# Performance work log

Measured on AMD Instinct MI355X. Metric: run time of the kernel, lower is better.

## Reference

```python
import jax, jax.numpy as jnp
import numpy as np

HEADS = 8
DK = 64            # key_size == size_per_head
NEIGHBORS = 3
KSIZE = 1 + 2 * NEIGHBORS  # 7 (rate=1)


def setup_inputs() -> dict:
    key = jax.random.key(0)
    k1, k2, k3, k4 = jax.random.split(key, 4)
    B, HW, S, D = 2, 64, 256, 512
    inputs = jax.random.normal(k1, (B, HW, S, D), dtype=jnp.float32)
    pos_bias = jax.random.normal(k2, (HEADS, S, KSIZE), dtype=jnp.float32)
    W_qkv = jax.random.normal(k3, (D, 3 * HEADS * DK), dtype=jnp.float32) * 0.02
    W_out = jax.random.normal(k4, (HEADS * DK, D), dtype=jnp.float32) * 0.02
    return {"inputs": inputs, "pos_bias": pos_bias, "W_qkv": W_qkv, "W_out": W_out}


def reference(inputs, pos_bias, W_qkv, W_out):
    B, HW, S, D = inputs.shape
    # qkv projection (no bias), split into q, k, v
    qkv = inputs @ W_qkv                                   # [B,HW,S,3*H*DK]
    q, k, v = jnp.split(qkv, 3, axis=-1)
    q = (q / jnp.sqrt(jnp.float32(DK))).reshape(B, HW, S, HEADS, DK)
    k = k.reshape(B, HW, S, HEADS, DK)
    v = v.reshape(B, HW, S, HEADS, DK)

    # zero-pad keys/values along seq (faithful to F.pad with value=0)
    pad = NEIGHBORS
    kp = jnp.pad(k, ((0, 0), (0, 0), (pad, pad), (0, 0), (0, 0)))
    vp = jnp.pad(v, ((0, 0), (0, 0), (pad, pad), (0, 0), (0, 0)))

    # sliding-window gather: window w for query i covers padded positions i..i+KSIZE-1
    idx = jnp.arange(S)[:, None] + jnp.arange(KSIZE)[None, :]  # [S,KSIZE]
    kw = kp[:, :, idx]                                         # [B,HW,S,KSIZE,H,DK]
    vw = vp[:, :, idx]                                         # [B,HW,S,KSIZE,H,DK]

    # scores over the window
    attn = jnp.einsum('bnshd,bnswhd->bnswh', q, kw)            # [B,HW,S,KSIZE,H]
    # additive positional bias: [H,S,KSIZE] -> [S,KSIZE,H] broadcast
    attn = attn + jnp.transpose(pos_bias, (1, 2, 0))[None, None]
    attn = jax.nn.softmax(attn, axis=-2)                       # softmax over window dim

    out = jnp.einsum('bnswh,bnswhd->bnshd', attn, vw)          # [B,HW,S,H,DK]
    out = out.reshape(B, HW, S, HEADS * DK)
    return out @ W_out
```

## Files before the change

kernel.cpp:

```cpp
#include <hip/hip_runtime.h>
#include <hip/hip_bf16.h>
#include <cstdint>


typedef __bf16 bf16x8 __attribute__((ext_vector_type(8)));
typedef float f32x4 __attribute__((ext_vector_type(4)));

__device__ __forceinline__ uint16_t f2bf(float f) {
    uint32_t u = __builtin_bit_cast(uint32_t, f);
    return (uint16_t)((u + 0x7fffu + ((u >> 16) & 1u)) >> 16);
}
__device__ __forceinline__ float bflo(uint32_t u) { return __builtin_bit_cast(float, u << 16); }
__device__ __forceinline__ float bfhi(uint32_t u) { return __builtin_bit_cast(float, u & 0xffff0000u); }

__device__ __forceinline__ void unpack8(uint4 v, float* f) {
    f[0] = bflo(v.x); f[1] = bfhi(v.x);
    f[2] = bflo(v.y); f[3] = bfhi(v.y);
    f[4] = bflo(v.z); f[5] = bfhi(v.z);
    f[6] = bflo(v.w); f[7] = bfhi(v.w);
}
__device__ __forceinline__ uint32_t pack2(float a, float b) {
    return (uint32_t)f2bf(a) | ((uint32_t)f2bf(b) << 16);
}

#define GLOAD_LDS16(gp, lp)                                                        \
    __builtin_amdgcn_global_load_lds((const __attribute__((address_space(1))) void*)(gp), \
                                     (__attribute__((address_space(3))) void*)(lp), 16, 0, 0)

__global__ void cvt_f32_bf16(const float* __restrict__ in, uint16_t* __restrict__ out, int n8) {
    int i = blockIdx.x * 256 + threadIdx.x;
    if (i >= n8) return;
    const float4* p = (const float4*)in + (size_t)i * 2;
    float4 a = p[0], b = p[1];
    uint4 o;
    o.x = pack2(a.x, a.y);
    o.y = pack2(a.z, a.w);
    o.z = pack2(b.x, b.y);
    o.w = pack2(b.z, b.w);
    *((uint4*)out + i) = o;
}

__global__ void transpose_cvt(const float* __restrict__ in, uint16_t* __restrict__ out,
                              int R, int C) {
    int idx = blockIdx.x * 256 + threadIdx.x;
    if (idx >= R * C) return;
    int r = idx / C;
    int c = idx - r * C;
    out[(size_t)c * R + r] = f2bf(in[idx]);
}

template <bool F32OUT>
__global__ __launch_bounds__(256, 2)
void gemm_bt(const uint16_t* __restrict__ A, const uint16_t* __restrict__ BT,
             void* __restrict__ Cout, int M, int N, int K) {
    __shared__ __align__(16) uint16_t As[128 * 32];
    __shared__ __align__(16) uint16_t Bs[128 * 32];

    const int tid  = threadIdx.x;
    const int lane = tid & 63;
    const int wv   = tid >> 6;
    const int r    = lane & 15;
    const int quad = lane >> 4;
    const int m_w  = (wv & 1) << 6;
    const int n_w  = (wv >> 1) << 6;
    const long bm0 = (long)blockIdx.x * 128;
    const long bn0 = (long)blockIdx.y * 128;

    f32x4 acc[4][4];
#pragma unroll
    for (int i = 0; i < 4; ++i)
#pragma unroll
        for (int j = 0; j < 4; ++j) acc[i][j] = (f32x4){0.f, 0.f, 0.f, 0.f};

    const int c0 = tid, c1 = tid + 256;
    const uint16_t* pA0 = A + (bm0 + (c0 >> 2)) * (long)K + (c0 & 3) * 8;
    const uint16_t* pA1 = A + (bm0 + (c1 >> 2)) * (long)K + (c1 & 3) * 8;
    const uint16_t* pB0 = BT + (bn0 + (c0 >> 2)) * (long)K + (c0 & 3) * 8;
    const uint16_t* pB1 = BT + (bn0 + (c1 >> 2)) * (long)K + (c1 & 3) * 8;

    for (int kt = 0; kt < K; kt += 32) {
        GLOAD_LDS16(pA0 + kt, &As[c0 * 8]);
        GLOAD_LDS16(pA1 + kt, &As[c1 * 8]);
        GLOAD_LDS16(pB0 + kt, &Bs[c0 * 8]);
        GLOAD_LDS16(pB1 + kt, &Bs[c1 * 8]);
        __syncthreads();

        bf16x8 af[4], bf[4];
#pragma unroll
        for (int mt = 0; mt < 4; ++mt)
            af[mt] = *(const bf16x8*)&As[(m_w + mt * 16 + r) * 32 + quad * 8];
#pragma unroll
        for (int nt = 0; nt < 4; ++nt)
            bf[nt] = *(const bf16x8*)&Bs[(n_w + nt * 16 + r) * 32 + quad * 8];
#pragma unroll
        for (int mt = 0; mt < 4; ++mt)
#pragma unroll
            for (int nt = 0; nt < 4; ++nt)
                acc[mt][nt] = __builtin_amdgcn_mfma_f32_16x16x32_bf16(af[mt], bf[nt],
                                                                      acc[mt][nt], 0, 0, 0);
        __syncthreads();
    }

#pragma unroll
    for (int mt = 0; mt < 4; ++mt) {
#pragma unroll
        for (int i = 0; i < 4; ++i) {
            long m = bm0 + m_w + mt * 16 + quad * 4 + i;
            if (F32OUT) {
                float* crow = (float*)Cout + m * (long)N + bn0 + n_w + r;
#pragma unroll
                for (int nt = 0; nt < 4; ++nt) crow[nt * 16] = acc[mt][nt][i];
            } else {
                uint16_t* crow = (uint16_t*)Cout + m * (long)N + bn0 + n_w + r;
#pragma unroll
                for (int nt = 0; nt < 4; ++nt) crow[nt * 16] = f2bf(acc[mt][nt][i]);
            }
        }
    }
}

__global__ __launch_bounds__(256, 2)
void local_attn(const uint16_t* __restrict__ qkv, const float* __restrict__ pb,
                uint16_t* __restrict__ attn) {
    __shared__ uint4 smem[4096];

    const int h  = blockIdx.x & 7;
    const int bn = blockIdx.x >> 3;
    const int s  = threadIdx.x;
    const size_t base = (size_t)bn * 256 * 1536;

#pragma unroll
    for (int it = 0; it < 16; ++it) {
        int i   = threadIdx.x + it * 256;
        int a   = i >> 11;
        int idx = i & 2047;
        int sp  = idx >> 3;
        int c8  = idx & 7;
        const uint16_t* src = qkv + base + (size_t)sp * 1536 + 512 + a * 512 + h * 64 + c8 * 8;
        smem[a * 2048 + sp * 8 + (c8 ^ (sp & 7))] = *(const uint4*)src;
    }

    const uint16_t* qrow = qkv + base + (size_t)s * 1536 + h * 64;
    uint4 qc[8];
#pragma unroll
    for (int c = 0; c < 8; ++c) qc[c] = *(const uint4*)(qrow + c * 8);

    __syncthreads();

    float sc[7];
#pragma unroll
    for (int w = 0; w < 7; ++w) sc[w] = 0.f;

#pragma unroll
    for (int c = 0; c < 8; ++c) {
        float qf[8];
        unpack8(qc[c], qf);
#pragma unroll
        for (int w = 0; w < 7; ++w) {
            int sp = s + w - 3;
            if ((unsigned)sp < 256u) {
                uint4 kc = smem[sp * 8 + (c ^ (sp & 7))];
                float kf[8];
                unpack8(kc, kf);
#pragma unroll
                for (int j = 0; j < 8; ++j) sc[w] += qf[j] * kf[j];
            }
        }
    }

    const float* pbr = pb + ((size_t)h * 256 + s) * 7;
    float mx = -1e30f;
#pragma unroll
    for (int w = 0; w < 7; ++w) {
        sc[w] = sc[w] * 0.125f + pbr[w];
        mx = fmaxf(mx, sc[w]);
    }
    float p[7], sum = 0.f;
#pragma unroll
    for (int w = 0; w < 7; ++w) {
        p[w] = __expf(sc[w] - mx);
        sum += p[w];
    }
    const float inv = 1.f / sum;
#pragma unroll
    for (int w = 0; w < 7; ++w) p[w] *= inv;

    uint4 ov[8];
#pragma unroll
    for (int c = 0; c < 8; ++c) {
        float o[8] = {0.f, 0.f, 0.f, 0.f, 0.f, 0.f, 0.f, 0.f};
#pragma unroll
        for (int w = 0; w < 7; ++w) {
            int sp = s + w - 3;
            if ((unsigned)sp < 256u) {
                uint4 vc = smem[2048 + sp * 8 + (c ^ (sp & 7))];
                float vf[8];
                unpack8(vc, vf);
#pragma unroll
                for (int j = 0; j < 8; ++j) o[j] += p[w] * vf[j];
            }
        }
        ov[c].x = pack2(o[0], o[1]);
        ov[c].y = pack2(o[2], o[3]);
        ov[c].z = pack2(o[4], o[5]);
        ov[c].w = pack2(o[6], o[7]);
    }

    uint16_t* orow = attn + ((size_t)(bn * 256 + s)) * 512 + h * 64;
#pragma unroll
    for (int c = 0; c < 8; ++c) *(uint4*)(orow + c * 8) = ov[c];
}

extern "C" void kernel_launch(void* const* d_in, const int* in_sizes, int n_in,
                              void* d_out, int out_size, void* d_ws, size_t ws_size,
                              hipStream_t stream) {
    const float* X    = (const float*)d_in[0];
    const float* pb   = (const float*)d_in[1];
    const float* Wqkv = (const float*)d_in[2];
    const float* Wout = (const float*)d_in[3];
    float* out = (float*)d_out;

    char* ws = (char*)d_ws;
    uint16_t* WqkvT = (uint16_t*)(ws);
    uint16_t* WoutT = (uint16_t*)(ws + 1572864);
    uint16_t* qkvb  = (uint16_t*)(ws + 2097152);
    uint16_t* Xb    = (uint16_t*)(ws + 102760448);
    uint16_t* attnb = Xb;

    cvt_f32_bf16<<<(32768 * 512 / 8 + 255) / 256, 256, 0, stream>>>(X, Xb, 32768 * 512 / 8);
    transpose_cvt<<<(512 * 1536 + 255) / 256, 256, 0, stream>>>(Wqkv, WqkvT, 512, 1536);
    transpose_cvt<<<(512 * 512 + 255) / 256, 256, 0, stream>>>(Wout, WoutT, 512, 512);

    gemm_bt<false><<<dim3(256, 12), 256, 0, stream>>>(Xb, WqkvT, qkvb, 32768, 1536, 512);
    local_attn<<<1024, 256, 0, stream>>>(qkvb, pb, attnb);
    gemm_bt<true><<<dim3(256, 4), 256, 0, stream>>>(attnb, WoutT, out, 32768, 512, 512);
}
```

Before: 266.8 us.

## Replace GEMM with 256x256 tile, double-buffered swizzled LDS pipelined kernel

Replaces the 128x128 single-buffered bf16 MFMA GEMM with a 256x256-tile, 512-thread kernel. It uses 64-wide K steps, XOR-swizzled LDS layout, double buffering with global_load_lds prefetch interleaved between MFMA phases, and setprio around the MFMA bursts. The goal is to hide global load latency, cut LDS bank conflicts and raise data reuse per tile. The cost is 128KB of LDS per block, which limits occupancy, and fewer blocks for the N=512 output GEMM (256 blocks).

```diff
diff --git a/kernel.cpp b/kernel.cpp
--- a/kernel.cpp
+++ b/kernel.cpp
@@ -50,73 +50,139 @@
 }
 
 template <bool F32OUT>
-__global__ __launch_bounds__(256, 2)
-void gemm_bt(const uint16_t* __restrict__ A, const uint16_t* __restrict__ BT,
+__global__ __launch_bounds__(512, 2)
+void gemm256(const uint16_t* __restrict__ A, const uint16_t* __restrict__ BT,
              void* __restrict__ Cout, int M, int N, int K) {
-    __shared__ __align__(16) uint16_t As[128 * 32];
-    __shared__ __align__(16) uint16_t Bs[128 * 32];
+    __shared__ __align__(16) uint16_t lds[65536];
 
     const int tid  = threadIdx.x;
     const int lane = tid & 63;
     const int wv   = tid >> 6;
     const int r    = lane & 15;
     const int quad = lane >> 4;
-    const int m_w  = (wv & 1) << 6;
-    const int n_w  = (wv >> 1) << 6;
-    const long bm0 = (long)blockIdx.x * 128;
-    const long bn0 = (long)blockIdx.y * 128;
-
-    f32x4 acc[4][4];
-#pragma unroll
-    for (int i = 0; i < 4; ++i)
-#pragma unroll
-        for (int j = 0; j < 4; ++j) acc[i][j] = (f32x4){0.f, 0.f, 0.f, 0.f};
-
-    const int c0 = tid, c1 = tid + 256;
-    const uint16_t* pA0 = A + (bm0 + (c0 >> 2)) * (long)K + (c0 & 3) * 8;
-    const uint16_t* pA1 = A + (bm0 + (c1 >> 2)) * (long)K + (c1 & 3) * 8;
-    const uint16_t* pB0 = BT + (bn0 + (c0 >> 2)) * (long)K + (c0 & 3) * 8;
-    const uint16_t* pB1 = BT + (bn0 + (c1 >> 2)) * (long)K + (c1 & 3) * 8;
-
-    for (int kt = 0; kt < K; kt += 32) {
-        GLOAD_LDS16(pA0 + kt, &As[c0 * 8]);
-        GLOAD_LDS16(pA1 + kt, &As[c1 * 8]);
-        GLOAD_LDS16(pB0 + kt, &Bs[c0 * 8]);
-        GLOAD_LDS16(pB1 + kt, &Bs[c1 * 8]);
-        __syncthreads();
-
-        bf16x8 af[4], bf[4];
-#pragma unroll
-        for (int mt = 0; mt < 4; ++mt)
-            af[mt] = *(const bf16x8*)&As[(m_w + mt * 16 + r) * 32 + quad * 8];
-#pragma unroll
-        for (int nt = 0; nt < 4; ++nt)
-            bf[nt] = *(const bf16x8*)&Bs[(n_w + nt * 16 + r) * 32 + quad * 8];
-#pragma unroll
-        for (int mt = 0; mt < 4; ++mt)
-#pragma unroll
-            for (int nt = 0; nt < 4; ++nt)
-                acc[mt][nt] = __builtin_amdgcn_mfma_f32_16x16x32_bf16(af[mt], bf[nt],
-                                                                      acc[mt][nt], 0, 0, 0);
-        __syncthreads();
-    }
-
-#pragma unroll
-    for (int mt = 0; mt < 4; ++mt) {
+    const int wr   = wv >> 2;
+    const int wc   = wv & 3;
+    const long bm0 = (long)blockIdx.x * 256;
+    const long bn0 = (long)blockIdx.y * 256;
+    const int NT   = K >> 6;
+
+    const int c0 = tid, c1 = tid + 512;
+    const int row0 = c0 >> 3, row1 = c1 >> 3;
+    const int sw0 = ((c0 & 7) ^ (row0 & 7)) * 8;
+    const int sw1 = ((c1 & 7) ^ (row1 & 7)) * 8;
+    const uint16_t* pA0 = A  + (bm0 + row0) * (long)K + sw0;
+    const uint16_t* pA1 = A  + (bm0 + row1) * (long)K + sw1;
+    const uint16_t* pB0 = BT + (bn0 + row0) * (long)K + sw0;
+    const uint16_t* pB1 = BT + (bn0 + row1) * (long)K + sw1;
+    const long hstep = 128 * (long)K;
+
+#define STAGE_A(b_, h_, t_) do {                                                        \
+        GLOAD_LDS16(pA0 + (h_) * hstep + (t_) * 64,                                     \
+                    &lds[(b_) * 16384 + (h_) * 8192 + c0 * 8]);                         \
+        GLOAD_LDS16(pA1 + (h_) * hstep + (t_) * 64,                                     \
+                    &lds[(b_) * 16384 + (h_) * 8192 + c1 * 8]);                         \
+    } while (0)
+#define STAGE_B(b_, h_, t_) do {                                                        \
+        GLOAD_LDS16(pB0 + (h_) * hstep + (t_) * 64,                                     \
+                    &lds[32768 + (b_) * 16384 + (h_) * 8192 + c0 * 8]);                 \
+        GLOAD_LDS16(pB1 + (h_) * hstep + (t_) * 64,                                     \
+                    &lds[32768 + (b_) * 16384 + (h_) * 8192 + c1 * 8]);                 \
+    } while (0)
+
+    const int swk0 = ((0 + quad) ^ (r & 7)) * 8;
+    const int swk1 = ((4 + quad) ^ (r & 7)) * 8;
+    const int arow = (wr * 128 + r) * 64;
+    const int brow = (wc * 64 + r) * 64;
+
+#define DS_A(mf_, kk_) (*(const bf16x8*)&lds[aoff + arow + (mf_) * 1024 + ((kk_) ? swk1 : swk0)])
+#define DS_B(nf_, kk_) (*(const bf16x8*)&lds[boff + brow + (nf_) * 1024 + ((kk_) ? swk1 : swk0)])
+
+    f32x4 acc[8][4];
+#pragma unroll
+    for (int mf = 0; mf < 8; ++mf)
+#pragma unroll
+        for (int nf = 0; nf < 4; ++nf) acc[mf][nf] = (f32x4){0.f, 0.f, 0.f, 0.f};
+
+    STAGE_A(0, 0, 0); STAGE_A(0, 1, 0);
+    STAGE_B(0, 0, 0); STAGE_B(0, 1, 0);
+    STAGE_B(1, 0, 1); STAGE_B(1, 1, 1);
+    asm volatile("s_waitcnt vmcnt(4)" ::: "memory");
+    __builtin_amdgcn_s_barrier();
+
+#define MFMA_PHASE(mbase_)                                                              \
+    __builtin_amdgcn_s_barrier();                                                       \
+    asm volatile("s_waitcnt lgkmcnt(0)");                                               \
+    __builtin_amdgcn_s_setprio(1);                                                      \
+    _Pragma("unroll")                                                                   \
+    for (int kk = 0; kk < 2; ++kk)                                                      \
+        _Pragma("unroll")                                                               \
+        for (int mi = 0; mi < 2; ++mi)                                                  \
+            _Pragma("unroll")                                                           \
+            for (int nf = 0; nf < 4; ++nf)                                              \
+                acc[(mbase_) + mi][nf] = __builtin_amdgcn_mfma_f32_16x16x32_bf16(       \
+                    af[mi][kk], bfr[nf][kk], acc[(mbase_) + mi][nf], 0, 0, 0);          \
+    __builtin_amdgcn_s_setprio(0);
+
+    for (int t = 0; t < NT; ++t) {
+        const int b    = t & 1;
+        const int aoff = b * 16384;
+        const int boff = 32768 + b * 16384;
+
+        bf16x8 bfr[4][2];
+        bf16x8 af[2][2];
+
+#pragma unroll
+        for (int nf = 0; nf < 4; ++nf) { bfr[nf][0] = DS_B(nf, 0); bfr[nf][1] = DS_B(nf, 1); }
+        af[0][0] = DS_A(0, 0); af[0][1] = DS_A(0, 1);
+        af[1][0] = DS_A(1, 0); af[1][1] = DS_A(1, 1);
+        if (t + 1 < NT) STAGE_A(b ^ 1, 0, t + 1);
+        MFMA_PHASE(0)
+        __builtin_amdgcn_s_barrier();
+
+        af[0][0] = DS_A(2, 0); af[0][1] = DS_A(2, 1);
+        af[1][0] = DS_A(3, 0); af[1][1] = DS_A(3, 1);
+        if (t + 1 < NT) STAGE_A(b ^ 1, 1, t + 1);
+        MFMA_PHASE(2)
+        __builtin_amdgcn_s_barrier();
+
+        af[0][0] = DS_A(4, 0); af[0][1] = DS_A(4, 1);
+        af[1][0] = DS_A(5, 0); af[1][1] = DS_A(5, 1);
+        if (t + 2 < NT) STAGE_B(b, 0, t + 2);
+        MFMA_PHASE(4)
+        __builtin_amdgcn_s_barrier();
+
+        af[0][0] = DS_A(6, 0); af[0][1] = DS_A(6, 1);
+        af[1][0] = DS_A(7, 0); af[1][1] = DS_A(7, 1);
+        if (t + 2 < NT) STAGE_B(b, 1, t + 2);
+        MFMA_PHASE(6)
+        if (t + 1 < NT) {
+            if (t + 2 < NT) asm volatile("s_waitcnt vmcnt(4)" ::: "memory");
+            else            asm volatile("s_waitcnt vmcnt(0)" ::: "memory");
+            __builtin_amdgcn_s_barrier();
+        }
+    }
+
+#pragma unroll
+    for (int mf = 0; mf < 8; ++mf) {
 #pragma unroll
         for (int i = 0; i < 4; ++i) {
-            long m = bm0 + m_w + mt * 16 + quad * 4 + i;
+            long m = bm0 + wr * 128 + mf * 16 + quad * 4 + i;
             if (F32OUT) {
-                float* crow = (float*)Cout + m * (long)N + bn0 + n_w + r;
-#pragma unroll
-                for (int nt = 0; nt < 4; ++nt) crow[nt * 16] = acc[mt][nt][i];
+                float* crow = (float*)Cout + m * (long)N + bn0 + wc * 64 + r;
+#pragma unroll
+                for (int nf = 0; nf < 4; ++nf) crow[nf * 16] = acc[mf][nf][i];
             } else {
-                uint16_t* crow = (uint16_t*)Cout + m * (long)N + bn0 + n_w + r;
-#pragma unroll
-                for (int nt = 0; nt < 4; ++nt) crow[nt * 16] = f2bf(acc[mt][nt][i]);
+                uint16_t* crow = (uint16_t*)Cout + m * (long)N + bn0 + wc * 64 + r;
+#pragma unroll
+                for (int nf = 0; nf < 4; ++nf) crow[nf * 16] = f2bf(acc[mf][nf][i]);
             }
         }
     }
+#undef STAGE_A
+#undef STAGE_B
+#undef DS_A
+#undef DS_B
+#undef MFMA_PHASE
 }
 
 __global__ __launch_bounds__(256, 2)
@@ -231,7 +297,7 @@
     transpose_cvt<<<(512 * 1536 + 255) / 256, 256, 0, stream>>>(Wqkv, WqkvT, 512, 1536);
     transpose_cvt<<<(512 * 512 + 255) / 256, 256, 0, stream>>>(Wout, WoutT, 512, 512);
 
-    gemm_bt<false><<<dim3(256, 12), 256, 0, stream>>>(Xb, WqkvT, qkvb, 32768, 1536, 512);
+    gemm256<false><<<dim3(128, 6), 512, 0, stream>>>(Xb, WqkvT, qkvb, 32768, 1536, 512);
     local_attn<<<1024, 256, 0, stream>>>(qkvb, pb, attnb);
-    gemm_bt<true><<<dim3(256, 4), 256, 0, stream>>>(attnb, WoutT, out, 32768, 512, 512);
-}
+    gemm256<true><<<dim3(128, 2), 512, 0, stream>>>(attnb, WoutT, out, 32768, 512, 512);
+}
```

New measurement: 263.9 us. No clear change (-1.1%).
